# Optimization experiments

Measured on AMD Instinct MI355X. Metric: run time of the kernel, lower is better.

The kernel has to match this reference:

```python
import jax, jax.numpy as jnp
import numpy as np

N_NODES = 200000
N_EDGES = 6400000
N_GRAPHS = 1000


def setup_inputs() -> dict:
    key = jax.random.key(0)
    ks = jax.random.split(key, 8)
    x = jax.random.normal(ks[0], (N_NODES, 2), dtype=jnp.float32)
    edge_index = jax.random.randint(ks[1], (2, N_EDGES), 0, N_NODES, dtype=jnp.int32)
    batch = jnp.sort(jax.random.randint(ks[2], (N_NODES,), 0, N_GRAPHS, dtype=jnp.int32))
    W1 = jax.random.normal(ks[3], (2, 16), dtype=jnp.float32) * (1.0 / np.sqrt(2))
    b1 = jnp.zeros((16,), jnp.float32)
    W2 = jax.random.normal(ks[4], (16, 32), dtype=jnp.float32) * (1.0 / np.sqrt(16))
    b2 = jnp.zeros((32,), jnp.float32)
    Wfc1 = jax.random.normal(ks[5], (32, 16), dtype=jnp.float32) * (1.0 / np.sqrt(32))
    bfc1 = jnp.zeros((16,), jnp.float32)
    Wfc2 = jax.random.normal(ks[6], (16, 1), dtype=jnp.float32) * (1.0 / np.sqrt(16))
    bfc2 = jnp.zeros((1,), jnp.float32)
    return {"x": x, "edge_index": edge_index, "batch": batch,
            "W1": W1, "b1": b1, "W2": W2, "b2": b2,
            "Wfc1": Wfc1, "bfc1": bfc1, "Wfc2": Wfc2, "bfc2": bfc2}


def _gcn_norm(edge_index, n_nodes):
    # PyG GCNConv default: add self loops, symmetric normalization.
    loops = jnp.arange(n_nodes, dtype=edge_index.dtype)
    src = jnp.concatenate([edge_index[0], loops])  # message source (row)
    dst = jnp.concatenate([edge_index[1], loops])  # aggregation target (col)
    deg = jax.ops.segment_sum(jnp.ones_like(dst, jnp.float32), dst, num_segments=n_nodes)
    dinv = jnp.where(deg > 0, jax.lax.rsqrt(jnp.maximum(deg, 1.0)), 0.0)
    norm = dinv[src] * dinv[dst]  # [E + N]
    return src, dst, norm


def _gcn_conv(h, W, b, src, dst, norm, n_nodes):
    h = h @ W                                      # transform first (small width)
    msg = h[src] * norm[:, None]                   # gather + scale: [E+N, F]
    out = jax.ops.segment_sum(msg, dst, num_segments=n_nodes)
    return out + b


def reference(x, edge_index, batch, W1, b1, W2, b2, Wfc1, bfc1, Wfc2, bfc2):
    n = x.shape[0]
    src, dst, norm = _gcn_norm(edge_index, n)
    h = jax.nn.relu(_gcn_conv(x, W1, b1, src, dst, norm, n))
    h = jax.nn.relu(_gcn_conv(h, W2, b2, src, dst, norm, n))
    # global_mean_pool over graph ids
    sums = jax.ops.segment_sum(h, batch, num_segments=N_GRAPHS)
    cnts = jax.ops.segment_sum(jnp.ones((n,), h.dtype), batch, num_segments=N_GRAPHS)
    pooled = sums / jnp.maximum(cnts, 1.0)[:, None]  # [G, 32]
    out = jax.nn.relu(pooled @ Wfc1 + bfc1)
    out = out @ Wfc2 + bfc2                          # [G, 1]
    return out.squeeze(-1)
```

## Files before the change

kernel.cpp:

```cpp
#include <hip/hip_runtime.h>
#include <hip/hip_fp16.h>

static inline size_t align256(size_t x) { return (x + 255) & ~size_t(255); }

#define CAP 36864

__global__ __launch_bounds__(1024) void k_scatter(const int* __restrict__ ei,
                                                  int* __restrict__ bcursor,
                                                  unsigned* __restrict__ bdata, int E) {
    __shared__ int lcount[256];
    __shared__ int gbase[256];
    int t = threadIdx.x;
    if (t < 256) lcount[t] = 0;
    __syncthreads();
    int chunk = blockIdx.x * 16384;
    int srcv[16], bkt[16], rank[16], dl[16];
#pragma unroll
    for (int k = 0; k < 8; ++k) {
        int e = chunk + k * 2048 + 2 * t;
        int k2 = 2 * k;
        bkt[k2] = -1; bkt[k2 + 1] = -1;
        if (e < E) {
            int2 sp = *(const int2*)(ei + e);
            int2 dp = *(const int2*)(ei + E + e);
            srcv[k2] = sp.x; bkt[k2] = dp.x >> 10; dl[k2] = dp.x & 1023;
            rank[k2] = atomicAdd(&lcount[bkt[k2]], 1);
            srcv[k2 + 1] = sp.y; bkt[k2 + 1] = dp.y >> 10; dl[k2 + 1] = dp.y & 1023;
            rank[k2 + 1] = atomicAdd(&lcount[bkt[k2 + 1]], 1);
        }
    }
    __syncthreads();
    if (t < 256) {
        int c = lcount[t];
        gbase[t] = t * CAP + (c ? atomicAdd(&bcursor[t], c) : 0);
    }
    __syncthreads();
#pragma unroll
    for (int k = 0; k < 16; ++k) {
        if (bkt[k] >= 0)
            bdata[gbase[bkt[k]] + rank[k]] = ((unsigned)dl[k] << 18) | (unsigned)srcv[k];
    }
}

__global__ __launch_bounds__(1024) void k_build(const unsigned* __restrict__ bdata,
                                                const int* __restrict__ bcursor,
                                                int* __restrict__ row_ptr,
                                                float* __restrict__ dinv,
                                                int* __restrict__ col,
                                                const float* __restrict__ x,
                                                float2* __restrict__ xt,
                                                int N, int E, int NBv) {
    __shared__ int curs[1024];
    __shared__ int sums[256];
    __shared__ int bsc[256];
    __shared__ int stage[CAP];
    int* hist = stage;
    int bkt = blockIdx.x;
    int t = threadIdx.x;
    if (t < 256) bsc[t] = (t < NBv) ? bcursor[t] : 0;
    __syncthreads();
    for (int off = 1; off < 256; off <<= 1) {
        int xv = 0;
        if (t < 256 && t >= off) xv = bsc[t - off];
        __syncthreads();
        if (t < 256) bsc[t] += xv;
        __syncthreads();
    }
    int count = bcursor[bkt];
    int tb = bsc[bkt] - count;
    int fs = bkt * CAP;
    int node0 = bkt << 10;
    int nn = N - node0; if (nn > 1024) nn = 1024;
    hist[t] = 0;
    __syncthreads();
    for (int e = t; e < count; e += 1024)
        atomicAdd(&hist[bdata[fs + e] >> 18], 1);
    __syncthreads();
    int v0 = 0, v1 = 0, v2 = 0, v3 = 0, s = 0;
    if (t < 256) {
        int b4 = t * 4;
        v0 = hist[b4]; v1 = hist[b4 + 1]; v2 = hist[b4 + 2]; v3 = hist[b4 + 3];
        s = v0 + v1 + v2 + v3;
        sums[t] = s;
    }
    __syncthreads();
    for (int off = 1; off < 256; off <<= 1) {
        int xv = 0;
        if (t < 256 && t >= off) xv = sums[t - off];
        __syncthreads();
        if (t < 256) sums[t] += xv;
        __syncthreads();
    }
    if (t < 256) {
        int b4 = t * 4;
        int e0 = sums[t] - s;
        int e1 = e0 + v0, e2 = e1 + v1, e3 = e2 + v2;
        curs[b4] = e0; curs[b4 + 1] = e1; curs[b4 + 2] = e2; curs[b4 + 3] = e3;
        if (b4 < nn)     { row_ptr[node0 + b4]     = tb + e0; dinv[node0 + b4]     = rsqrtf((float)v0 + 1.f); }
        if (b4 + 1 < nn) { row_ptr[node0 + b4 + 1] = tb + e1; dinv[node0 + b4 + 1] = rsqrtf((float)v1 + 1.f); }
        if (b4 + 2 < nn) { row_ptr[node0 + b4 + 2] = tb + e2; dinv[node0 + b4 + 2] = rsqrtf((float)v2 + 1.f); }
        if (b4 + 3 < nn) { row_ptr[node0 + b4 + 3] = tb + e3; dinv[node0 + b4 + 3] = rsqrtf((float)v3 + 1.f); }
    }
    if (bkt == NBv - 1 && t == 0) row_ptr[N] = E;
    __syncthreads();
    for (int e = t; e < count; e += 1024) {
        unsigned p = bdata[fs + e];
        int dl = p >> 18;
        int pos = atomicAdd(&curs[dl], 1);
        stage[pos] = (int)(p & 0x3FFFFu);
    }
    __syncthreads();
    for (int i = t; i < count; i += 1024)
        col[tb + i] = stage[i];
    for (int i = t; i < nn; i += 1024) {
        int node = node0 + i;
        float d2 = dinv[node];
        xt[node] = make_float2(x[node * 2] * d2, x[node * 2 + 1] * d2);
    }
}

__global__ __launch_bounds__(256) void k_conv1_fused(const int* __restrict__ rp,
                                                     const int* __restrict__ col,
                                                     const float2* __restrict__ xt,
                                                     const float* __restrict__ dinv,
                                                     const float* __restrict__ W1,
                                                     const float* __restrict__ b1,
                                                     uint2* __restrict__ ht, int n) {
    int gt = blockIdx.x * 256 + threadIdx.x;
    int node = gt >> 2;
    int q = gt & 3;
    if (node >= n) return;
    int rs = rp[node], re = rp[node + 1];
    float a0 = 0.f, a1 = 0.f;
    int e = rs + q;
    for (; e + 12 < re; e += 16) {
        int c0 = __builtin_nontemporal_load(col + e);
        int c1 = __builtin_nontemporal_load(col + e + 4);
        int c2 = __builtin_nontemporal_load(col + e + 8);
        int c3 = __builtin_nontemporal_load(col + e + 12);
        float2 v0 = xt[c0];
        float2 v1 = xt[c1];
        float2 v2 = xt[c2];
        float2 v3 = xt[c3];
        a0 += (v0.x + v1.x) + (v2.x + v3.x);
        a1 += (v0.y + v1.y) + (v2.y + v3.y);
    }
    for (; e < re; e += 4) {
        float2 v = xt[__builtin_nontemporal_load(col + e)];
        a0 += v.x; a1 += v.y;
    }
    if (q == 0) { float2 sf = xt[node]; a0 += sf.x; a1 += sf.y; }
    a0 += __shfl_xor(a0, 1); a0 += __shfl_xor(a0, 2);
    a1 += __shfl_xor(a1, 1); a1 += __shfl_xor(a1, 2);
    float dv = dinv[node];
    a0 *= dv; a1 *= dv;
    int f0 = q * 4;
    float v0 = fmaxf(a0 * W1[f0]     + a1 * W1[16 + f0]     + b1[f0],     0.f) * dv;
    float v1 = fmaxf(a0 * W1[f0 + 1] + a1 * W1[16 + f0 + 1] + b1[f0 + 1], 0.f) * dv;
    float v2 = fmaxf(a0 * W1[f0 + 2] + a1 * W1[16 + f0 + 2] + b1[f0 + 2], 0.f) * dv;
    float v3 = fmaxf(a0 * W1[f0 + 3] + a1 * W1[16 + f0 + 3] + b1[f0 + 3], 0.f) * dv;
    __half2 h0 = __floats2half2_rn(v0, v1);
    __half2 h1 = __floats2half2_rn(v2, v3);
    uint2 w;
    w.x = *reinterpret_cast<unsigned*>(&h0);
    w.y = *reinterpret_cast<unsigned*>(&h1);
    ht[(size_t)node * 4 + q] = w;
}

__global__ __launch_bounds__(256) void k_gather2(const int* __restrict__ rp,
                                                 const int* __restrict__ col,
                                                 const __half2* __restrict__ ht,
                                                 const float* __restrict__ dinv,
                                                 float* __restrict__ agg, int N) {
    int gt = blockIdx.x * 256 + threadIdx.x;
    int node = gt >> 3;
    int fq = gt & 7;
    if (node >= N) return;
    int rs = rp[node], re = rp[node + 1];
    const __half2* __restrict__ base = ht + fq;
    float ax = 0.f, ay = 0.f;
    int e = rs;
    for (; e + 16 <= re; e += 16) {
        int c[16];
#pragma unroll
        for (int k = 0; k < 16; ++k) c[k] = __builtin_nontemporal_load(col + e + k);
        float2 v[16];
#pragma unroll
        for (int k = 0; k < 16; ++k) v[k] = __half22float2(base[(size_t)c[k] * 8]);
#pragma unroll
        for (int k = 0; k < 16; ++k) { ax += v[k].x; ay += v[k].y; }
    }
    for (; e + 8 <= re; e += 8) {
        int c[8];
#pragma unroll
        for (int k = 0; k < 8; ++k) c[k] = __builtin_nontemporal_load(col + e + k);
        float2 v[8];
#pragma unroll
        for (int k = 0; k < 8; ++k) v[k] = __half22float2(base[(size_t)c[k] * 8]);
#pragma unroll
        for (int k = 0; k < 8; ++k) { ax += v[k].x; ay += v[k].y; }
    }
    for (; e < re; ++e) {
        float2 v = __half22float2(base[(size_t)col[e] * 8]);
        ax += v.x; ay += v.y;
    }
    {
        float2 v = __half22float2(base[(size_t)node * 8]);
        ax += v.x; ay += v.y;
    }
    float dv = dinv[node];
    __builtin_nontemporal_store(ax * dv, agg + (size_t)node * 16 + 2 * fq);
    __builtin_nontemporal_store(ay * dv, agg + (size_t)node * 16 + 2 * fq + 1);
}

__global__ __launch_bounds__(256) void k_trans_pool(const float* __restrict__ agg,
                                                    const float* __restrict__ W2,
                                                    const float* __restrict__ b2,
                                                    const int* __restrict__ batch,
                                                    float* __restrict__ gsum, int N) {
    __shared__ float aggs[64][17];
    __shared__ float h2s[64][33];
    __shared__ float w2s[512];
    __shared__ float b2s[32];
    __shared__ int   bids[64];
    int t = threadIdx.x;
    if (t < 128) ((float4*)w2s)[t] = ((const float4*)W2)[t];
    if (t < 32)  b2s[t] = b2[t];
    int node0 = blockIdx.x * 64;
    if (t < 64)  bids[t] = (node0 + t < N) ? batch[node0 + t] : -1;
    {
        int nl = t >> 2, q = t & 3;
        int node = node0 + nl;
        float4 v = make_float4(0.f, 0.f, 0.f, 0.f);
        if (node < N) v = *(const float4*)(agg + (size_t)node * 16 + (size_t)q * 4);
        int c0 = q * 4;
        aggs[nl][c0] = v.x; aggs[nl][c0 + 1] = v.y;
        aggs[nl][c0 + 2] = v.z; aggs[nl][c0 + 3] = v.w;
    }
    __syncthreads();
    {
        int nl = t >> 2;
        int jq = (t & 3) * 8;
        float o[8];
#pragma unroll
        for (int j = 0; j < 8; ++j) o[j] = b2s[jq + j];
#pragma unroll
        for (int k = 0; k < 16; ++k) {
            float a = aggs[nl][k];
#pragma unroll
            for (int j = 0; j < 8; ++j) o[j] += a * w2s[k * 32 + jq + j];
        }
#pragma unroll
        for (int j = 0; j < 8; ++j) h2s[nl][jq + j] = fmaxf(o[j], 0.f);
    }
    __syncthreads();
    if (t < 128) {
        int j = t & 31, seg = t >> 5;
        int nbeg = seg * 16, nend = nbeg + 16;
        float acc = 0.f;
        int cur = bids[nbeg];
        for (int n2 = nbeg; n2 < nend; ++n2) {
            int b = bids[n2];
            if (b != cur) {
                if (cur >= 0) atomicAdd(&gsum[(size_t)cur * 32 + j], acc);
                acc = 0.f; cur = b;
            }
            if (b >= 0) acc += h2s[n2][j];
        }
        if (cur >= 0) atomicAdd(&gsum[(size_t)cur * 32 + j], acc);
    }
}

__global__ void k_final(const float* __restrict__ gsum, const int* __restrict__ batch,
                        const float* __restrict__ Wfc1, const float* __restrict__ bfc1,
                        const float* __restrict__ Wfc2, const float* __restrict__ bfc2,
                        float* __restrict__ out, int G, int N) {
    int g = blockIdx.x * blockDim.x + threadIdx.x;
    if (g >= G) return;
    int lo = 0, hi = N;
    while (lo < hi) { int m = (lo + hi) >> 1; if (batch[m] < g) lo = m + 1; else hi = m; }
    int s = lo;
    lo = s; hi = N;
    while (lo < hi) { int m = (lo + hi) >> 1; if (batch[m] < g + 1) lo = m + 1; else hi = m; }
    float cnt = (float)(lo - s);
    float inv = 1.f / fmaxf(cnt, 1.f);
    float p[32];
#pragma unroll
    for (int i = 0; i < 32; ++i) p[i] = gsum[(size_t)g * 32 + i] * inv;
    float o = bfc2[0];
#pragma unroll
    for (int j = 0; j < 16; ++j) {
        float a = bfc1[j];
#pragma unroll
        for (int i = 0; i < 32; ++i) a += p[i] * Wfc1[i * 16 + j];
        o += fmaxf(a, 0.f) * Wfc2[j];
    }
    out[g] = o;
}

extern "C" void kernel_launch(void* const* d_in, const int* in_sizes, int n_in,
                              void* d_out, int out_size, void* d_ws, size_t ws_size,
                              hipStream_t stream) {
    const float* x     = (const float*)d_in[0];
    const int*   ei    = (const int*)d_in[1];
    const int*   batch = (const int*)d_in[2];
    const float* W1    = (const float*)d_in[3];
    const float* b1    = (const float*)d_in[4];
    const float* W2    = (const float*)d_in[5];
    const float* b2    = (const float*)d_in[6];
    const float* Wfc1  = (const float*)d_in[7];
    const float* bfc1  = (const float*)d_in[8];
    const float* Wfc2  = (const float*)d_in[9];
    const float* bfc2  = (const float*)d_in[10];
    float* out = (float*)d_out;

    const int N = in_sizes[0] / 2;
    const int E = in_sizes[1] / 2;
    const int G = out_size;
    const int NBv = (N + 1023) >> 10;

    char* ws = (char*)d_ws;
    size_t off = 0;
    float* dinv    = (float*)(ws + off); off += align256((size_t)N * 4);
    int*   row_ptr = (int*)(ws + off);   off += align256((size_t)(N + 1) * 4);
    int*   bcursor = (int*)(ws + off);   size_t z0 = off; off += align256(256 * 4);
    float* gsum    = (float*)(ws + off); off += align256((size_t)G * 32 * 4);
    size_t zlen = off - z0;
    float2* xt     = (float2*)(ws + off); off += align256((size_t)N * 8);
    __half2* ht    = (__half2*)(ws + off); off += align256((size_t)N * 32);
    float* agg     = (float*)(ws + off); off += align256((size_t)N * 16 * 4);
    int*   col     = (int*)(ws + off);   off += align256((size_t)E * 4);
    unsigned* bdata = (unsigned*)(ws + off); off += align256((size_t)NBv * CAP * 4);

    const int BS = 256;

    hipMemsetAsync(bcursor, 0, zlen, stream);

    k_scatter<<<(E + 16383) / 16384, 1024, 0, stream>>>(ei, bcursor, bdata, E);
    k_build<<<NBv, 1024, 0, stream>>>(bdata, bcursor, row_ptr, dinv, col, x, xt, N, E, NBv);

    k_conv1_fused<<<((size_t)N * 4 + 255) / 256, 256, 0, stream>>>(row_ptr, col, xt, dinv,
                                                                   W1, b1, (uint2*)ht, N);
    k_gather2<<<((size_t)N * 8 + 255) / 256, 256, 0, stream>>>(row_ptr, col, ht, dinv, agg, N);
    k_trans_pool<<<(N + 63) / 64, 256, 0, stream>>>(agg, W2, b2, batch, gsum, N);

    k_final<<<(G + BS - 1) / BS, BS, 0, stream>>>(gsum, batch, Wfc1, bfc1, Wfc2, bfc2,
                                                  out, G, N);
}
```

Baseline: 244.4 us.

## Split layer-2 gather into two passes by source-node half for cache locality

```diff
diff --git a/kernel.cpp b/kernel.cpp
--- a/kernel.cpp
+++ b/kernel.cpp
@@ -45,16 +45,17 @@
 __global__ __launch_bounds__(1024) void k_build(const unsigned* __restrict__ bdata,
                                                 const int* __restrict__ bcursor,
                                                 int* __restrict__ row_ptr,
+                                                int* __restrict__ rmid,
                                                 float* __restrict__ dinv,
                                                 int* __restrict__ col,
                                                 const float* __restrict__ x,
                                                 float2* __restrict__ xt,
-                                                int N, int E, int NBv) {
-    __shared__ int curs[1024];
+                                                int N, int E, int NBv, int Nh) {
+    __shared__ int curs2[2048];
     __shared__ int sums[256];
     __shared__ int bsc[256];
     __shared__ int stage[CAP];
-    int* hist = stage;
+    int* hist2 = stage;
     int bkt = blockIdx.x;
     int t = threadIdx.x;
     if (t < 256) bsc[t] = (t < NBv) ? bcursor[t] : 0;
@@ -71,16 +72,20 @@
     int fs = bkt * CAP;
     int node0 = bkt << 10;
     int nn = N - node0; if (nn > 1024) nn = 1024;
-    hist[t] = 0;
-    __syncthreads();
-    for (int e = t; e < count; e += 1024)
-        atomicAdd(&hist[bdata[fs + e] >> 18], 1);
-    __syncthreads();
-    int v0 = 0, v1 = 0, v2 = 0, v3 = 0, s = 0;
+    hist2[t] = 0; hist2[t + 1024] = 0;
+    __syncthreads();
+    for (int e = t; e < count; e += 1024) {
+        unsigned p = bdata[fs + e];
+        int dl = p >> 18;
+        int half = ((int)(p & 0x3FFFFu) >= Nh) ? 1 : 0;
+        atomicAdd(&hist2[dl * 2 + half], 1);
+    }
+    __syncthreads();
+    int h[8], s = 0;
     if (t < 256) {
-        int b4 = t * 4;
-        v0 = hist[b4]; v1 = hist[b4 + 1]; v2 = hist[b4 + 2]; v3 = hist[b4 + 3];
-        s = v0 + v1 + v2 + v3;
+        int b8 = t * 8;
+#pragma unroll
+        for (int i = 0; i < 8; ++i) { h[i] = hist2[b8 + i]; s += h[i]; }
         sums[t] = s;
     }
     __syncthreads();
@@ -92,22 +97,31 @@
         __syncthreads();
     }
     if (t < 256) {
-        int b4 = t * 4;
-        int e0 = sums[t] - s;
-        int e1 = e0 + v0, e2 = e1 + v1, e3 = e2 + v2;
-        curs[b4] = e0; curs[b4 + 1] = e1; curs[b4 + 2] = e2; curs[b4 + 3] = e3;
-        if (b4 < nn)     { row_ptr[node0 + b4]     = tb + e0; dinv[node0 + b4]     = rsqrtf((float)v0 + 1.f); }
-        if (b4 + 1 < nn) { row_ptr[node0 + b4 + 1] = tb + e1; dinv[node0 + b4 + 1] = rsqrtf((float)v1 + 1.f); }
-        if (b4 + 2 < nn) { row_ptr[node0 + b4 + 2] = tb + e2; dinv[node0 + b4 + 2] = rsqrtf((float)v2 + 1.f); }
-        if (b4 + 3 < nn) { row_ptr[node0 + b4 + 3] = tb + e3; dinv[node0 + b4 + 3] = rsqrtf((float)v3 + 1.f); }
+        int b8 = t * 8;
+        int pos = sums[t] - s;
+#pragma unroll
+        for (int j = 0; j < 4; ++j) {
+            int nd = t * 4 + j;
+            int pLo = pos; pos += h[2 * j];
+            int pHi = pos; pos += h[2 * j + 1];
+            curs2[b8 + 2 * j] = pLo;
+            curs2[b8 + 2 * j + 1] = pHi;
+            if (nd < nn) {
+                row_ptr[node0 + nd] = tb + pLo;
+                rmid[node0 + nd]    = tb + pHi;
+                dinv[node0 + nd]    = rsqrtf((float)(h[2 * j] + h[2 * j + 1]) + 1.f);
+            }
+        }
     }
     if (bkt == NBv - 1 && t == 0) row_ptr[N] = E;
     __syncthreads();
     for (int e = t; e < count; e += 1024) {
         unsigned p = bdata[fs + e];
         int dl = p >> 18;
-        int pos = atomicAdd(&curs[dl], 1);
-        stage[pos] = (int)(p & 0x3FFFFu);
+        int src = (int)(p & 0x3FFFFu);
+        int half = (src >= Nh) ? 1 : 0;
+        int pos = atomicAdd(&curs2[dl * 2 + half], 1);
+        stage[pos] = src;
     }
     __syncthreads();
     for (int i = t; i < count; i += 1024)
@@ -167,16 +181,18 @@
     ht[(size_t)node * 4 + q] = w;
 }
 
-__global__ __launch_bounds__(256) void k_gather2(const int* __restrict__ rp,
-                                                 const int* __restrict__ col,
-                                                 const __half2* __restrict__ ht,
-                                                 const float* __restrict__ dinv,
-                                                 float* __restrict__ agg, int N) {
+__global__ __launch_bounds__(256) void k_gather2s(const int* __restrict__ rsArr,
+                                                  const int* __restrict__ reArr,
+                                                  const int* __restrict__ col,
+                                                  const __half2* __restrict__ ht,
+                                                  const float* __restrict__ dinv,
+                                                  float* __restrict__ agg, int N,
+                                                  int Nh, int passB) {
     int gt = blockIdx.x * 256 + threadIdx.x;
     int node = gt >> 3;
     int fq = gt & 7;
     if (node >= N) return;
-    int rs = rp[node], re = rp[node + 1];
+    int rs = rsArr[node], re = reArr[node];
     const __half2* __restrict__ base = ht + fq;
     float ax = 0.f, ay = 0.f;
     int e = rs;
@@ -204,7 +220,7 @@
         float2 v = __half22float2(base[(size_t)col[e] * 8]);
         ax += v.x; ay += v.y;
     }
-    {
+    if (((node >= Nh) ? 1 : 0) == passB) {
         float2 v = __half22float2(base[(size_t)node * 8]);
         ax += v.x; ay += v.y;
     }
@@ -213,7 +229,8 @@
     __builtin_nontemporal_store(ay * dv, agg + (size_t)node * 16 + 2 * fq + 1);
 }
 
-__global__ __launch_bounds__(256) void k_trans_pool(const float* __restrict__ agg,
+__global__ __launch_bounds__(256) void k_trans_pool(const float* __restrict__ aggA,
+                                                    const float* __restrict__ aggB,
                                                     const float* __restrict__ W2,
                                                     const float* __restrict__ b2,
                                                     const int* __restrict__ batch,
@@ -231,11 +248,17 @@
     {
         int nl = t >> 2, q = t & 3;
         int node = node0 + nl;
-        float4 v = make_float4(0.f, 0.f, 0.f, 0.f);
-        if (node < N) v = *(const float4*)(agg + (size_t)node * 16 + (size_t)q * 4);
+        float4 va = make_float4(0.f, 0.f, 0.f, 0.f);
+        float4 vb = make_float4(0.f, 0.f, 0.f, 0.f);
+        if (node < N) {
+            va = *(const float4*)(aggA + (size_t)node * 16 + (size_t)q * 4);
+            vb = *(const float4*)(aggB + (size_t)node * 16 + (size_t)q * 4);
+        }
         int c0 = q * 4;
-        aggs[nl][c0] = v.x; aggs[nl][c0 + 1] = v.y;
-        aggs[nl][c0 + 2] = v.z; aggs[nl][c0 + 3] = v.w;
+        aggs[nl][c0]     = va.x + vb.x;
+        aggs[nl][c0 + 1] = va.y + vb.y;
+        aggs[nl][c0 + 2] = va.z + vb.z;
+        aggs[nl][c0 + 3] = va.w + vb.w;
     }
     __syncthreads();
     {
@@ -318,17 +341,20 @@
     const int E = in_sizes[1] / 2;
     const int G = out_size;
     const int NBv = (N + 1023) >> 10;
+    const int Nh = N >> 1;
 
     char* ws = (char*)d_ws;
     size_t off = 0;
     float* dinv    = (float*)(ws + off); off += align256((size_t)N * 4);
     int*   row_ptr = (int*)(ws + off);   off += align256((size_t)(N + 1) * 4);
+    int*   rmid    = (int*)(ws + off);   off += align256((size_t)N * 4);
     int*   bcursor = (int*)(ws + off);   size_t z0 = off; off += align256(256 * 4);
     float* gsum    = (float*)(ws + off); off += align256((size_t)G * 32 * 4);
     size_t zlen = off - z0;
     float2* xt     = (float2*)(ws + off); off += align256((size_t)N * 8);
     __half2* ht    = (__half2*)(ws + off); off += align256((size_t)N * 32);
-    float* agg     = (float*)(ws + off); off += align256((size_t)N * 16 * 4);
+    float* aggA    = (float*)(ws + off); off += align256((size_t)N * 16 * 4);
+    float* aggB    = (float*)(ws + off); off += align256((size_t)N * 16 * 4);
     int*   col     = (int*)(ws + off);   off += align256((size_t)E * 4);
     unsigned* bdata = (unsigned*)(ws + off); off += align256((size_t)NBv * CAP * 4);
 
@@ -337,12 +363,15 @@
     hipMemsetAsync(bcursor, 0, zlen, stream);
 
     k_scatter<<<(E + 16383) / 16384, 1024, 0, stream>>>(ei, bcursor, bdata, E);
-    k_build<<<NBv, 1024, 0, stream>>>(bdata, bcursor, row_ptr, dinv, col, x, xt, N, E, NBv);
+    k_build<<<NBv, 1024, 0, stream>>>(bdata, bcursor, row_ptr, rmid, dinv, col, x, xt,
+                                      N, E, NBv, Nh);
 
     k_conv1_fused<<<((size_t)N * 4 + 255) / 256, 256, 0, stream>>>(row_ptr, col, xt, dinv,
                                                                    W1, b1, (uint2*)ht, N);
-    k_gather2<<<((size_t)N * 8 + 255) / 256, 256, 0, stream>>>(row_ptr, col, ht, dinv, agg, N);
-    k_trans_pool<<<(N + 63) / 64, 256, 0, stream>>>(agg, W2, b2, batch, gsum, N);
+    int gblk = ((size_t)N * 8 + 255) / 256;
+    k_gather2s<<<gblk, 256, 0, stream>>>(row_ptr, rmid, col, ht, dinv, aggA, N, Nh, 0);
+    k_gather2s<<<gblk, 256, 0, stream>>>(rmid, row_ptr + 1, col, ht, dinv, aggB, N, Nh, 1);
+    k_trans_pool<<<(N + 63) / 64, 256, 0, stream>>>(aggA, aggB, W2, b2, batch, gsum, N);
 
     k_final<<<(G + BS - 1) / BS, BS, 0, stream>>>(gsum, batch, Wfc1, bfc1, Wfc2, bfc2,
                                                   out, G, N);
```

New measurement: 258.9 us. +5.9%, slower.
